# Optimization experiments

Measured on AMD Instinct MI355X. Metric: run time of the kernel, lower is better.

The kernel has to match this reference:

```python
import jax, jax.numpy as jnp
import numpy as np

B_TREES, NARY, HS, NHEAD, NLVL = 16, 3, 512, 2, 6
EDIM = 352
LN_EPS = 1e-5

def _build_structure():
    # forest of B_TREES perfect ternary trees, depth NLVL; nodes numbered leaves-first, level-major
    off, o = {}, 0
    for l in range(NLVL - 1, -1, -1):
        off[l] = o
        o += B_TREES * 3 ** l
    node_ids = [off[l] + np.arange(B_TREES * 3 ** l) for l in range(NLVL)]
    child_idx = {}
    for l in range(NLVL - 1):
        m = 3 ** l
        t = np.repeat(np.arange(B_TREES), m)
        p = np.tile(np.arange(m), B_TREES)
        base = off[l + 1] + t * (3 ** (l + 1)) + 3 * p
        child_idx[l] = base[:, None] + np.arange(NARY)[None, :]
    return o, node_ids, child_idx

N_NODES, NODE_IDS, CHILD_IDX = _build_structure()

def _ln(x, w, b):
    mu = x.mean(-1, keepdims=True)
    var = x.var(-1, keepdims=True)
    return (x - mu) / jnp.sqrt(var + LN_EPS) * w + b

def _mha(x, wqkv, bqkv, wo, bo):
    # x: [S, B, H]; torch MHA with batch_first=False (seq dim 0, as in reduce_func)
    S, B, H = x.shape
    hd = H // NHEAD
    q, k, v = jnp.split(x @ wqkv.T + bqkv, 3, axis=-1)
    q = q.reshape(S, B, NHEAD, hd)
    k = k.reshape(S, B, NHEAD, hd)
    v = v.reshape(S, B, NHEAD, hd)
    scores = jnp.einsum('sbnd,tbnd->bnst', q, k) / jnp.sqrt(jnp.asarray(hd, x.dtype))
    attn = jax.nn.softmax(scores, axis=-1)
    o = jnp.einsum('bnst,tbnd->sbnd', attn, v).reshape(S, B, H)
    return o @ wo.T + bo

def _transformer(x, qkv_w, qkv_b, out_w, out_b, ln1_w, ln1_b, ff1_w, ff1_b, ff2_w, ff2_b, ln2_w, ln2_b):
    # 2 post-norm TransformerEncoderLayers, relu FF, dropout off (eval)
    for i in range(2):
        x = _ln(x + _mha(x, qkv_w[i], qkv_b[i], out_w[i], out_b[i]), ln1_w[i], ln1_b[i])
        ff = jax.nn.relu(x @ ff1_w[i].T + ff1_b[i]) @ ff2_w[i].T + ff2_b[i]
        x = _ln(x + ff, ln2_w[i], ln2_b[i])
    return x

def _forward(floats, ints):
    (user_emb, poi_emb, cat_emb, coo_emb, time_pos, W_iou, U_iou, b_iou,
     W_f, U_f, b_f, qkv_w, qkv_b, out_w, out_b, ln1_w, ln1_b, ff1_w, ff1_b,
     ff2_w, ff2_b, ln2_w, ln2_b, dec_poi_w, dec_poi_b, dec_cat_w, dec_cat_b,
     dec_coo_w, dec_coo_b) = floats
    user_ids, poi_ids, cat_ids, coo_ids, time_ids, mask = ints
    mi = mask.astype(jnp.int32)
    x = jnp.concatenate([user_emb[user_ids * mi], poi_emb[poi_ids * mi],
                         cat_emb[cat_ids * mi], coo_emb[coo_ids * mi]], axis=1)
    x = x + 0.5 * time_pos[time_ids * mi]
    x = x * mask.astype(x.dtype)[:, None]  # embed_dropout is identity in eval; per-node mask
    h = jnp.zeros((N_NODES, HS), x.dtype)
    c = jnp.zeros((N_NODES, HS), x.dtype)
    # leaves: reduce never fires -> iou stays at W_iou(x) (no b_iou), c = 0
    leaf = NODE_IDS[NLVL - 1]
    i0, o0, u0 = jnp.split(x[leaf] @ W_iou.T, 3, axis=1)
    c_leaf = jax.nn.sigmoid(i0) * jnp.tanh(u0)
    h = h.at[leaf].set(jax.nn.sigmoid(o0) * jnp.tanh(c_leaf))
    c = c.at[leaf].set(c_leaf)
    # topological propagation, bottom-up level frontiers
    for l in range(NLVL - 2, -1, -1):
        idx = NODE_IDS[l]
        ci = CHILD_IDX[l]
        m = idx.shape[0]
        h_ch = h[ci]  # mailbox gather [m, nary, HS]
        c_ch = c[ci]
        xl = x[idx]
        Wx = jnp.tile(xl @ W_f.T, (1, NARY))
        f = jax.nn.sigmoid(Wx + h_ch.reshape(m, NARY * HS) @ U_f.T + jnp.tile(b_f, (1, NARY)))
        h_att = _transformer(h_ch, qkv_w, qkv_b, out_w, out_b, ln1_w, ln1_b,
                             ff1_w, ff1_b, ff2_w, ff2_b, ln2_w, ln2_b)
        iou = xl @ W_iou.T + h_att.reshape(m, NARY * HS) @ U_iou.T + b_iou
        c_red = jnp.sum(f.reshape(m, NARY, HS) * c_ch, axis=1)
        i1, o1, u1 = jnp.split(iou, 3, axis=1)
        c_new = jax.nn.sigmoid(i1) * jnp.tanh(u1) + c_red
        h_new = jax.nn.sigmoid(o1) * jnp.tanh(c_new)
        h = h.at[idx].set(h_new)
        c = c.at[idx].set(c_new)
    # model_dropout identity in eval
    y_poi = h @ dec_poi_w.T + dec_poi_b
    y_cat = h @ dec_cat_w.T + dec_cat_b
    y_coo = h @ dec_coo_w.T + dec_coo_b
    return y_poi, y_cat, y_coo

def setup_inputs():
    key = jax.random.key(0)
    ks = iter(jax.random.split(key, 64))
    def rn(shape, s=0.05):
        return jax.random.normal(next(ks), shape, dtype=jnp.float32) * s
    def ri(shape, hi):
        return jax.random.randint(next(ks), shape, 0, hi, dtype=jnp.int32)
    N = N_NODES
    return dict(
        user_ids=ri([N], 3000), poi_ids=ri([N], 5000), cat_ids=ri([N], 300),
        coo_ids=ri([N], 1024), time_ids=ri([N], 96), mask=ri([N], 2),
        user_emb=rn([3000, 128], 0.02), poi_emb=rn([5000, 128], 0.02),
        cat_emb=rn([300, 32], 0.02), coo_emb=rn([1024, 64], 0.02),
        time_pos=rn([96, EDIM], 0.02),
        W_iou=rn([3 * HS, EDIM]), U_iou=rn([3 * HS, NARY * HS]), b_iou=jnp.zeros((1, 3 * HS)),
        W_f=rn([HS, EDIM]), U_f=rn([NARY * HS, NARY * HS]), b_f=jnp.zeros((1, HS)),
        qkv_w=rn([2, 3 * HS, HS]), qkv_b=jnp.zeros((2, 3 * HS)),
        out_w=rn([2, HS, HS]), out_b=jnp.zeros((2, HS)),
        ln1_w=jnp.ones((2, HS)), ln1_b=jnp.zeros((2, HS)),
        ff1_w=rn([2, HS, HS]), ff1_b=jnp.zeros((2, HS)),
        ff2_w=rn([2, HS, HS]), ff2_b=jnp.zeros((2, HS)),
        ln2_w=jnp.ones((2, HS)), ln2_b=jnp.zeros((2, HS)),
        dec_poi_w=rn([5000, HS]), dec_poi_b=jnp.zeros((5000,)),
        dec_cat_w=rn([300, HS]), dec_cat_b=jnp.zeros((300,)),
        dec_coo_w=rn([1024, HS]), dec_coo_b=jnp.zeros((1024,)),
    )

def reference(user_ids, poi_ids, cat_ids, coo_ids, time_ids, mask,
              user_emb, poi_emb, cat_emb, coo_emb, time_pos,
              W_iou, U_iou, b_iou, W_f, U_f, b_f,
              qkv_w, qkv_b, out_w, out_b, ln1_w, ln1_b, ff1_w, ff1_b,
              ff2_w, ff2_b, ln2_w, ln2_b,
              dec_poi_w, dec_poi_b, dec_cat_w, dec_cat_b, dec_coo_w, dec_coo_b):
    floats = (user_emb, poi_emb, cat_emb, coo_emb, time_pos, W_iou, U_iou, b_iou,
              W_f, U_f, b_f, qkv_w, qkv_b, out_w, out_b, ln1_w, ln1_b, ff1_w, ff1_b,
              ff2_w, ff2_b, ln2_w, ln2_b, dec_poi_w, dec_poi_b, dec_cat_w, dec_cat_b,
              dec_coo_w, dec_coo_b)
    ints = (user_ids, poi_ids, cat_ids, coo_ids, time_ids, mask)
    return _forward(floats, ints)
```

## Files before the change

### kernel.cpp

```cpp
#include <hip/hip_runtime.h>
#include <hip/hip_bf16.h>


namespace {

constexpr int NN = 5824;
constexpr int ED = 352;

typedef __bf16 bf16;
typedef short s16x8 __attribute__((ext_vector_type(8)));
typedef float f32x4 __attribute__((ext_vector_type(4)));

__device__ __forceinline__ float sigmoidf_(float x) { return 1.f / (1.f + expf(-x)); }

__device__ __forceinline__ void gload_lds16(const void* g, void* s) {
  __builtin_amdgcn_global_load_lds(
      (const __attribute__((address_space(1))) unsigned int*)g,
      (__attribute__((address_space(3))) unsigned int*)s, 16, 0, 0);
}

template <int MODE>
__global__ __launch_bounds__(256) void bgemm_k(
    const bf16* __restrict__ A, const bf16* __restrict__ Alo, const bf16* __restrict__ B,
    void* __restrict__ Cp, bf16* __restrict__ Clo, const float* __restrict__ Cacc,
    const float* __restrict__ bias, int M, int N, int K, int lda, int ldb, int ldc,
    float alpha, long long sA1, long long sA2, long long sB1, long long sB2,
    long long sC1, long long sC2, int nh) {
  constexpr bool DUAL = (MODE == 1 || MODE == 2 || MODE == 4 || MODE == 5 || MODE == 6);
  const int bz = blockIdx.z;
  const int b1 = bz / nh, b2 = bz - b1 * nh;
  A += (long long)b1 * sA1 + (long long)b2 * sA2;
  if (DUAL) Alo += (long long)b1 * sA1 + (long long)b2 * sA2;
  B += (long long)b1 * sB1 + (long long)b2 * sB2;
  const long long coff = (long long)b1 * sC1 + (long long)b2 * sC2;
  const int bm = blockIdx.y * 128, bn = blockIdx.x * 128;
  __shared__ bf16 As[128 * 32];
  __shared__ bf16 Ls[DUAL ? 128 * 32 : 8];
  __shared__ bf16 Bs[128 * 32];
  const int tid = threadIdx.x;
  const int l = tid & 63;
  const int wr = ((tid >> 7) & 1) * 64;
  const int wc = ((tid >> 6) & 1) * 64;
  f32x4 acc[4][4];
#pragma unroll
  for (int i = 0; i < 4; ++i)
#pragma unroll
    for (int j = 0; j < 4; ++j) acc[i][j] = (f32x4){0.f, 0.f, 0.f, 0.f};

  for (int k0 = 0; k0 < K; k0 += 32) {
#pragma unroll
    for (int r = 0; r < 2; ++r) {
      int idx = r * 256 + tid;
      int row = idx >> 2, cs = idx & 3;
      int cg = cs ^ (row & 3);
      int ra = bm + row; if (ra > M - 1) ra = M - 1;
      int rb = bn + row; if (rb > N - 1) rb = N - 1;
      gload_lds16(A + (long long)ra * lda + k0 + cg * 8, As + idx * 8);
      if (DUAL) gload_lds16(Alo + (long long)ra * lda + k0 + cg * 8, Ls + idx * 8);
      gload_lds16(B + (long long)rb * ldb + k0 + cg * 8, Bs + idx * 8);
    }
    __syncthreads();
    s16x8 af[4], al[4], bfr[4];
#pragma unroll
    for (int mi = 0; mi < 4; ++mi) {
      int row = wr + mi * 16 + (l & 15);
      int ch = ((l >> 4) ^ row) & 3;
      af[mi] = *reinterpret_cast<const s16x8*>(As + row * 32 + ch * 8);
      if (DUAL) al[mi] = *reinterpret_cast<const s16x8*>(Ls + row * 32 + ch * 8);
    }
#pragma unroll
    for (int ni = 0; ni < 4; ++ni) {
      int row = wc + ni * 16 + (l & 15);
      int ch = ((l >> 4) ^ row) & 3;
      bfr[ni] = *reinterpret_cast<const s16x8*>(Bs + row * 32 + ch * 8);
    }
#pragma unroll
    for (int mi = 0; mi < 4; ++mi)
#pragma unroll
      for (int ni = 0; ni < 4; ++ni) {
        acc[mi][ni] =
            __builtin_amdgcn_mfma_f32_16x16x32_bf16(af[mi], bfr[ni], acc[mi][ni], 0, 0, 0);
        if (DUAL)
          acc[mi][ni] =
              __builtin_amdgcn_mfma_f32_16x16x32_bf16(al[mi], bfr[ni], acc[mi][ni], 0, 0, 0);
      }
    __syncthreads();
  }

  const int lc = l & 15, lr4 = (l >> 4) * 4;
#pragma unroll
  for (int mi = 0; mi < 4; ++mi) {
#pragma unroll
    for (int j = 0; j < 4; ++j) {
      int r = bm + wr + mi * 16 + lr4 + j;
      if (r >= M) continue;
#pragma unroll
      for (int ni = 0; ni < 4; ++ni) {
        int c = bn + wc + ni * 16 + lc;
        if (c >= N) continue;
        float v = alpha * acc[mi][ni][j];
        if (bias) v += bias[c];
        long long idx = coff + (long long)r * ldc + c;
        if (MODE == 5) v += Cacc[idx];
        if (MODE == 0 || MODE == 1 || MODE == 5) {
          ((float*)Cp)[idx] = v;
        } else if (MODE == 2 || MODE == 3) {
          ((bf16*)Cp)[idx] = (bf16)v;
        } else if (MODE == 4) {
          v = fmaxf(v, 0.f);
          bf16 hv = (bf16)v;
          ((bf16*)Cp)[idx] = hv;
          Clo[idx] = (bf16)(v - (float)hv);
        } else {
          float* o0 = (float*)Cp;
          if (c < 5000)      o0[(long long)r * 5000 + c] = v;
          else if (c < 5300) o0[29120000LL + (long long)r * 300 + (c - 5000)] = v;
          else               o0[30867200LL + (long long)r * 1024 + (c - 5300)] = v;
        }
      }
    }
  }
}

static void bgemm(hipStream_t st, int mode, const bf16* A, const bf16* Alo, const bf16* B,
                  void* Cp, bf16* Clo, const float* Cacc, const float* bias,
                  int M, int N, int K, int lda, int ldb, int ldc, float alpha,
                  int batches = 1, long long sA1 = 0, long long sA2 = 0, long long sB1 = 0,
                  long long sB2 = 0, long long sC1 = 0, long long sC2 = 0, int nh = 1) {
  dim3 g((N + 127) / 128, (M + 127) / 128, batches), b(256);
#define BGL(MD_)                                                                          \
  bgemm_k<MD_><<<g, b, 0, st>>>(A, Alo, B, Cp, Clo, Cacc, bias, M, N, K, lda, ldb, ldc,   \
                                alpha, sA1, sA2, sB1, sB2, sC1, sC2, nh)
  switch (mode) {
    case 0: BGL(0); break;
    case 1: BGL(1); break;
    case 2: BGL(2); break;
    case 3: BGL(3); break;
    case 4: BGL(4); break;
    case 5: BGL(5); break;
    default: BGL(6); break;
  }
#undef BGL
}

__global__ __launch_bounds__(256) void cvt8_k(const float* __restrict__ s,
                                              bf16* __restrict__ d, int n8) {
  int i = blockIdx.x * 256 + threadIdx.x;
  if (i >= n8) return;
  const float4* p = reinterpret_cast<const float4*>(s + (long long)i * 8);
  float4 a = p[0], b = p[1];
  bf16 o[8] = {(bf16)a.x, (bf16)a.y, (bf16)a.z, (bf16)a.w,
               (bf16)b.x, (bf16)b.y, (bf16)b.z, (bf16)b.w};
  *reinterpret_cast<s16x8*>(d + (long long)i * 8) = *reinterpret_cast<s16x8*>(o);
}

__global__ __launch_bounds__(256) void biascat_k(const float* __restrict__ p,
                                                 const float* __restrict__ c,
                                                 const float* __restrict__ g,
                                                 float* __restrict__ o) {
  int i = blockIdx.x * 256 + threadIdx.x;
  if (i >= 6324) return;
  o[i] = (i < 5000) ? p[i] : (i < 5300) ? c[i - 5000] : g[i - 5300];
}

__global__ __launch_bounds__(256) void embed_k(
    const int* __restrict__ uid, const int* __restrict__ pid, const int* __restrict__ cid,
    const int* __restrict__ gid, const int* __restrict__ tmid, const int* __restrict__ mask,
    const float* __restrict__ ue, const float* __restrict__ pe, const float* __restrict__ ce,
    const float* __restrict__ ge, const float* __restrict__ tp, bf16* __restrict__ xb) {
  int e = blockIdx.x * 256 + threadIdx.x;
  if (e >= NN * ED) return;
  int n = e / ED, j = e - n * ED;
  int mi = mask[n];
  float fm = (float)mi;
  float v;
  if (j < 128)      v = ue[(long long)(uid[n] * mi) * 128 + j];
  else if (j < 256) v = pe[(long long)(pid[n] * mi) * 128 + (j - 128)];
  else if (j < 288) v = ce[(long long)(cid[n] * mi) * 32 + (j - 256)];
  else              v = ge[(long long)(gid[n] * mi) * 64 + (j - 288)];
  v += 0.5f * tp[(long long)(tmid[n] * mi) * ED + j];
  xb[e] = (bf16)(v * fm);
}

__global__ __launch_bounds__(256) void gather_k(
    const bf16* __restrict__ hhi, const bf16* __restrict__ hlo, const float* __restrict__ c,
    bf16* __restrict__ ghi, bf16* __restrict__ glo, float* __restrict__ cch,
    int m, int cbase, int tl) {
  int e = blockIdx.x * 256 + threadIdx.x;
  if (e >= m * 1536) return;
  int r = e / 1536, rem = e - r * 1536;
  int k = rem >> 9, d = rem & 511;
  int t = r / tl, p = r - t * tl;
  long long src = (long long)(cbase + t * 3 * tl + 3 * p + k) * 512 + d;
  ghi[e] = hhi[src];
  glo[e] = hlo[src];
  cch[e] = c[src];
}

__global__ __launch_bounds__(256) void fcred_k(
    const float* __restrict__ wx, const float* __restrict__ ufh, const float* __restrict__ bf_,
    const float* __restrict__ cch, float* __restrict__ cred, int m) {
  int e = blockIdx.x * 256 + threadIdx.x;
  if (e >= m * 512) return;
  int r = e >> 9, d = e & 511;
  float w = wx[e] + bf_[d];
  long long base = (long long)r * 1536;
  float acc = 0.f;
#pragma unroll
  for (int k = 0; k < 3; ++k) {
    float f = sigmoidf_(w + ufh[base + k * 512 + d]);
    acc += f * cch[base + k * 512 + d];
  }
  cred[e] = acc;
}

__global__ __launch_bounds__(256) void combine_k(
    const float* __restrict__ iou, const float* __restrict__ cred, float* __restrict__ c,
    bf16* __restrict__ hhi, bf16* __restrict__ hlo, int off, int m) {
  int e = blockIdx.x * 256 + threadIdx.x;
  if (e >= m * 512) return;
  int r = e >> 9, d = e & 511;
  long long b = (long long)r * 1536;
  float iv = iou[b + d], ov = iou[b + 512 + d], uv = iou[b + 1024 + d];
  float cr = cred ? cred[e] : 0.f;
  float cn = sigmoidf_(iv) * tanhf(uv) + cr;
  float hn = sigmoidf_(ov) * tanhf(cn);
  long long o = (long long)(off + r) * 512 + d;
  c[o] = cn;
  bf16 hv = (bf16)hn;
  hhi[o] = hv;
  hlo[o] = (bf16)(hn - (float)hv);
}

__global__ __launch_bounds__(256) void ln_k(
    const bf16* __restrict__ ahi, const bf16* __restrict__ alo, const float* __restrict__ b,
    const float* __restrict__ w, const float* __restrict__ bias,
    bf16* __restrict__ ohi, bf16* __restrict__ olo) {
  int r = blockIdx.x, t = threadIdx.x;
  long long base = (long long)r * 512;
  float v0 = (float)ahi[base + t] + (float)alo[base + t] + b[base + t];
  float v1 = (float)ahi[base + 256 + t] + (float)alo[base + 256 + t] + b[base + 256 + t];
  __shared__ float s1[256], s2[256];
  s1[t] = v0 + v1;
  s2[t] = v0 * v0 + v1 * v1;
  __syncthreads();
  for (int s = 128; s > 0; s >>= 1) {
    if (t < s) { s1[t] += s1[t + s]; s2[t] += s2[t + s]; }
    __syncthreads();
  }
  float mu = s1[0] * (1.f / 512.f);
  float var = s2[0] * (1.f / 512.f) - mu * mu;
  float rs = rsqrtf(var + 1e-5f);
  float o0 = (v0 - mu) * rs * w[t] + bias[t];
  float o1 = (v1 - mu) * rs * w[256 + t] + bias[256 + t];
  bf16 h0 = (bf16)o0, h1 = (bf16)o1;
  ohi[base + t] = h0;       olo[base + t] = (bf16)(o0 - (float)h0);
  ohi[base + 256 + t] = h1; olo[base + 256 + t] = (bf16)(o1 - (float)h1);
}

__global__ __launch_bounds__(256) void softmax_pb_k(
    const float* __restrict__ sc, bf16* __restrict__ pb, int m, int mpad) {
  long long r = blockIdx.x;
  const float* row = sc + r * m;
  bf16* prow = pb + r * mpad;
  int t = threadIdx.x;
  __shared__ float sh[256];
  float mx = -3.4e38f;
  for (int j = t; j < m; j += 256) mx = fmaxf(mx, row[j]);
  sh[t] = mx;
  __syncthreads();
  for (int s = 128; s > 0; s >>= 1) {
    if (t < s) sh[t] = fmaxf(sh[t], sh[t + s]);
    __syncthreads();
  }
  mx = sh[0];
  __syncthreads();
  float sum = 0.f;
  for (int j = t; j < m; j += 256) sum += expf(row[j] - mx);
  sh[t] = sum;
  __syncthreads();
  for (int s = 128; s > 0; s >>= 1) {
    if (t < s) sh[t] += sh[t + s];
    __syncthreads();
  }
  float inv = 1.f / sh[0];
  for (int j = t; j < mpad; j += 256)
    prow[j] = (j < m) ? (bf16)(expf(row[j] - mx) * inv) : (bf16)0.f;
}

__global__ __launch_bounds__(256) void vt_k(const bf16* __restrict__ qkvb,
                                            bf16* __restrict__ vt, int m, int mpad) {
  int total = 6 * 256 * mpad;
  for (int e = blockIdx.x * 256 + threadIdx.x; e < total; e += gridDim.x * 256) {
    int z = e / (256 * mpad);
    int rem = e - z * 256 * mpad;
    int n = rem / mpad, k = rem - n * mpad;
    int b = z >> 1, h = z & 1;
    bf16 v = (bf16)0.f;
    if (k < m) v = qkvb[(long long)(k * 3 + b) * 1536 + 1024 + h * 256 + n];
    vt[e] = v;
  }
}

}

extern "C" void kernel_launch(void* const* d_in, const int* in_sizes, int n_in,
                              void* d_out, int out_size, void* d_ws, size_t ws_size,
                              hipStream_t stream) {
  const int* uid  = (const int*)d_in[0];
  const int* pid  = (const int*)d_in[1];
  const int* cid  = (const int*)d_in[2];
  const int* gid  = (const int*)d_in[3];
  const int* tmid = (const int*)d_in[4];
  const int* mask = (const int*)d_in[5];
  const float* ue = (const float*)d_in[6];
  const float* pe = (const float*)d_in[7];
  const float* ce = (const float*)d_in[8];
  const float* ge = (const float*)d_in[9];
  const float* tp = (const float*)d_in[10];
  const float* W_iou = (const float*)d_in[11];
  const float* U_iou = (const float*)d_in[12];
  const float* b_iou = (const float*)d_in[13];
  const float* W_f = (const float*)d_in[14];
  const float* U_f = (const float*)d_in[15];
  const float* b_f = (const float*)d_in[16];
  const float* qkv_w = (const float*)d_in[17];
  const float* qkv_b = (const float*)d_in[18];
  const float* out_w = (const float*)d_in[19];
  const float* out_b = (const float*)d_in[20];
  const float* ln1_w = (const float*)d_in[21];
  const float* ln1_b = (const float*)d_in[22];
  const float* ff1_w = (const float*)d_in[23];
  const float* ff1_b = (const float*)d_in[24];
  const float* ff2_w = (const float*)d_in[25];
  const float* ff2_b = (const float*)d_in[26];
  const float* ln2_w = (const float*)d_in[27];
  const float* ln2_b = (const float*)d_in[28];
  const float* dpw = (const float*)d_in[29];
  const float* dpb = (const float*)d_in[30];
  const float* dcw = (const float*)d_in[31];
  const float* dcb = (const float*)d_in[32];
  const float* dgw = (const float*)d_in[33];
  const float* dgb = (const float*)d_in[34];

  float* ws = (float*)d_ws;
  bf16* Hhi = (bf16*)ws;
  bf16* Hlo = Hhi + 2981888LL;
  bf16* dwcat = (bf16*)(ws + 2981888LL);
  float* bcat = ws + 4600832LL;

  float* ob = (float*)d_out;
  float* R1   = ob;
  float* PQ   = ob + 10077696LL;
  bf16* VT    = (bf16*)(ob + 15178752LL);
  bf16* ATTOb = (bf16*)(ob + 16186368LL);
  float* SCR  = ob + 17181696LL;
  bf16* XChi  = (bf16*)(ob + 19172352LL);
  bf16* XClo  = XChi + 1990656LL;
  bf16* RAhi  = (bf16*)(ob + 21163008LL);
  bf16* RAlo  = RAhi + 1990656LL;
  bf16* RBhi  = (bf16*)(ob + 23153664LL);
  bf16* RBlo  = RBhi + 1990656LL;
  float* WX   = ob + 25144320LL;
  float* CRED = ob + 25807872LL;
  float* Cc   = ob + 26471424LL;
  bf16* Xb    = (bf16*)(ob + 29453312LL);
  bf16* Wb    = (bf16*)(ob + 30478336LL);

  float* SC   = R1;
  float* IOU  = R1;
  bf16* QKVb  = (bf16*)PQ;
  float* UFH  = PQ;
  bf16* Pb    = (bf16*)PQ;
  float* CCH  = SCR;
  float* XB   = SCR;

  bf16* W_ioub = Wb;
  bf16* U_ioub = Wb + 540672LL;
  bf16* W_fb   = Wb + 2899968LL;
  bf16* U_fb   = Wb + 3080192LL;
  bf16* qkvb   = Wb + 5439488LL;
  bf16* outb   = Wb + 7012352LL;
  bf16* ff1b   = Wb + 7536640LL;
  bf16* ff2b   = Wb + 8060928LL;

#define CVT(src, dst, n) cvt8_k<<<((n) / 8 + 255) / 256, 256, 0, stream>>>(src, dst, (n) / 8)
  CVT(W_iou, W_ioub, 540672);
  CVT(U_iou, U_ioub, 2359296);
  CVT(W_f, W_fb, 180224);
  CVT(U_f, U_fb, 2359296);
  CVT(qkv_w, qkvb, 1572864);
  CVT(out_w, outb, 524288);
  CVT(ff1_w, ff1b, 524288);
  CVT(ff2_w, ff2b, 524288);
  CVT(dpw, dwcat, 2560000);
  CVT(dcw, dwcat + 2560000LL, 153600);
  CVT(dgw, dwcat + 2713600LL, 524288);
#undef CVT
  biascat_k<<<25, 256, 0, stream>>>(dpb, dcb, dgb, bcat);

  embed_k<<<(NN * ED + 255) / 256, 256, 0, stream>>>(uid, pid, cid, gid, tmid, mask,
                                                     ue, pe, ce, ge, tp, Xb);

  bgemm(stream, 0, Xb, nullptr, W_ioub, R1, nullptr, nullptr, nullptr,
        3888, 1536, 352, 352, 352, 1536, 1.f);
  combine_k<<<(3888 * 512 + 255) / 256, 256, 0, stream>>>(R1, nullptr, Cc, Hhi, Hlo, 0, 3888);

  static const int OFFL[6] = {5808, 5760, 5616, 5184, 3888, 0};
  int tl = 81;
  for (int l = 4; l >= 0; --l, tl /= 3) {
    int m = 16 * tl;
    int off = OFFL[l];
    int cbase = OFFL[l + 1];
    int T = 3 * m;
    int mpad = (m + 31) & ~31;
    const bf16* xlb = Xb + (long long)off * ED;

    gather_k<<<(m * 1536 + 255) / 256, 256, 0, stream>>>(Hhi, Hlo, Cc, RAhi, RAlo, CCH,
                                                         m, cbase, tl);
    bgemm(stream, 0, xlb, nullptr, W_fb, WX, nullptr, nullptr, nullptr,
          m, 512, 352, 352, 352, 512, 1.f);
    bgemm(stream, 1, RAhi, RAlo, U_fb, UFH, nullptr, nullptr, nullptr,
          m, 1536, 1536, 1536, 1536, 1536, 1.f);
    fcred_k<<<(m * 512 + 255) / 256, 256, 0, stream>>>(WX, UFH, b_f, CCH, CRED, m);

    bf16 *curhi = RAhi, *curlo = RAlo, *nxthi = RBhi, *nxtlo = RBlo;
    for (int i = 0; i < 2; ++i) {
      bgemm(stream, 2, curhi, curlo, qkvb + (long long)i * 786432, QKVb, nullptr, nullptr,
            qkv_b + i * 1536, T, 1536, 512, 512, 512, 1536, 1.f);
      {
        int total = 6 * 256 * mpad;
        int blocks = (total + 255) / 256; if (blocks > 2048) blocks = 2048;
        vt_k<<<blocks, 256, 0, stream>>>(QKVb, VT, m, mpad);
      }
      bgemm(stream, 0, QKVb, nullptr, QKVb + 512, SC, nullptr, nullptr, nullptr,
            m, m, 256, 4608, 4608, m, 0.0625f,
            6, 1536, 256, 1536, 256, 2LL * m * m, (long long)m * m, 2);
      softmax_pb_k<<<6 * m, 256, 0, stream>>>(SC, Pb, m, mpad);
      bgemm(stream, 3, Pb, nullptr, VT, ATTOb, nullptr, nullptr, nullptr,
            m, 256, mpad, mpad, mpad, 1536, 1.f,
            6, 2LL * m * mpad, (long long)m * mpad, 2LL * 256 * mpad, 256LL * mpad,
            512, 256, 2);
      bgemm(stream, 0, ATTOb, nullptr, outb + (long long)i * 262144, XB, nullptr, nullptr,
            out_b + i * 512, T, 512, 512, 512, 512, 512, 1.f);
      ln_k<<<T, 256, 0, stream>>>(curhi, curlo, XB, ln1_w + i * 512, ln1_b + i * 512,
                                  nxthi, nxtlo);
      bgemm(stream, 4, nxthi, nxtlo, ff1b + (long long)i * 262144, XChi, XClo, nullptr,
            ff1_b + i * 512, T, 512, 512, 512, 512, 512, 1.f);
      bgemm(stream, 1, XChi, XClo, ff2b + (long long)i * 262144, XB, nullptr, nullptr,
            ff2_b + i * 512, T, 512, 512, 512, 512, 512, 1.f);
      ln_k<<<T, 256, 0, stream>>>(nxthi, nxtlo, XB, ln2_w + i * 512, ln2_b + i * 512,
                                  curhi, curlo);
    }

    bgemm(stream, 0, xlb, nullptr, W_ioub, IOU, nullptr, nullptr, b_iou,
          m, 1536, 352, 352, 352, 1536, 1.f);
    bgemm(stream, 5, curhi, curlo, U_ioub, IOU, nullptr, IOU, nullptr,
          m, 1536, 1536, 1536, 1536, 1536, 1.f);
    combine_k<<<(m * 512 + 255) / 256, 256, 0, stream>>>(IOU, CRED, Cc, Hhi, Hlo, off, m);
  }

  bgemm(stream, 6, Hhi, Hlo, dwcat, ob, nullptr, nullptr, bcat,
        NN, 6324, 512, 512, 512, 0, 1.f);
}
```

Before: 2.417 ms.

## Convert fp32 weights inside GEMM tiles and fuse gather, V-transpose and batched projections

Drops the upfront weight conversion kernels. The GEMM now loads fp32 weights directly and splits them into hi/lo bf16 pairs, adding an extra MFMA per step for weight precision. The V transpose moves into the QKV GEMM epilogue, child gathering moves into combine_k and fcred_k, and the W_iou/W_f input projections run once for all nodes instead of per level. The decoder reads its three weight and bias tables directly, removing concatenation. This cuts launches and intermediate traffic, but the extra MFMAs and in-loop fp32 conversion add compute on every GEMM, including the large decoder GEMM.

```diff
diff --git a/kernel.cpp b/kernel.cpp
--- a/kernel.cpp
+++ b/kernel.cpp
@@ -19,24 +19,31 @@
       (__attribute__((address_space(3))) unsigned int*)s, 16, 0, 0);
 }
 
-template <int MODE>
+template <int MODE, int BSRC>
 __global__ __launch_bounds__(256) void bgemm_k(
-    const bf16* __restrict__ A, const bf16* __restrict__ Alo, const bf16* __restrict__ B,
+    const bf16* __restrict__ A, const bf16* __restrict__ Alo,
+    const bf16* __restrict__ Bb, const float* __restrict__ Bf,
+    const float* __restrict__ Bf0, const float* __restrict__ Bf1,
+    const float* __restrict__ Bf2,
     void* __restrict__ Cp, bf16* __restrict__ Clo, const float* __restrict__ Cacc,
-    const float* __restrict__ bias, int M, int N, int K, int lda, int ldb, int ldc,
-    float alpha, long long sA1, long long sA2, long long sB1, long long sB2,
+    const float* __restrict__ bias, const float* __restrict__ bias1,
+    const float* __restrict__ bias2, bf16* __restrict__ VTout, int mpad,
+    int M, int N, int K, int lda, int ldb, int ldc, float alpha,
+    long long sA1, long long sA2, long long sB1, long long sB2,
     long long sC1, long long sC2, int nh) {
-  constexpr bool DUAL = (MODE == 1 || MODE == 2 || MODE == 4 || MODE == 5 || MODE == 6);
+  constexpr bool DUAL = (MODE == 1 || MODE == 4 || MODE == 5 || MODE == 6 || MODE == 7);
+  constexpr bool WF = (BSRC >= 1);
   const int bz = blockIdx.z;
   const int b1 = bz / nh, b2 = bz - b1 * nh;
   A += (long long)b1 * sA1 + (long long)b2 * sA2;
   if (DUAL) Alo += (long long)b1 * sA1 + (long long)b2 * sA2;
-  B += (long long)b1 * sB1 + (long long)b2 * sB2;
+  if (BSRC == 0) Bb += (long long)b1 * sB1 + (long long)b2 * sB2;
   const long long coff = (long long)b1 * sC1 + (long long)b2 * sC2;
   const int bm = blockIdx.y * 128, bn = blockIdx.x * 128;
   __shared__ bf16 As[128 * 32];
   __shared__ bf16 Ls[DUAL ? 128 * 32 : 8];
-  __shared__ bf16 Bs[128 * 32];
+  __shared__ bf16 Bh[128 * 32];
+  __shared__ bf16 Bl[WF ? 128 * 32 : 8];
   const int tid = threadIdx.x;
   const int l = tid & 63;
   const int wr = ((tid >> 7) & 1) * 64;
@@ -57,10 +64,33 @@
       int rb = bn + row; if (rb > N - 1) rb = N - 1;
       gload_lds16(A + (long long)ra * lda + k0 + cg * 8, As + idx * 8);
       if (DUAL) gload_lds16(Alo + (long long)ra * lda + k0 + cg * 8, Ls + idx * 8);
-      gload_lds16(B + (long long)rb * ldb + k0 + cg * 8, Bs + idx * 8);
+      if (BSRC == 0) {
+        gload_lds16(Bb + (long long)rb * ldb + k0 + cg * 8, Bh + idx * 8);
+      } else {
+        const float* src;
+        if (BSRC == 2) {
+          if (rb < 5000)      src = Bf0 + (long long)rb * ldb + k0 + cg * 8;
+          else if (rb < 5300) src = Bf1 + (long long)(rb - 5000) * ldb + k0 + cg * 8;
+          else                src = Bf2 + (long long)(rb - 5300) * ldb + k0 + cg * 8;
+        } else {
+          src = Bf + (long long)rb * ldb + k0 + cg * 8;
+        }
+        float4 x = *reinterpret_cast<const float4*>(src);
+        float4 y = *reinterpret_cast<const float4*>(src + 4);
+        float w[8] = {x.x, x.y, x.z, x.w, y.x, y.y, y.z, y.w};
+        bf16 hb_[8], lb_[8];
+#pragma unroll
+        for (int q = 0; q < 8; ++q) {
+          bf16 hq = (bf16)w[q];
+          hb_[q] = hq;
+          lb_[q] = (bf16)(w[q] - (float)hq);
+        }
+        *reinterpret_cast<s16x8*>(Bh + idx * 8) = *reinterpret_cast<s16x8*>(hb_);
+        *reinterpret_cast<s16x8*>(Bl + idx * 8) = *reinterpret_cast<s16x8*>(lb_);
+      }
     }
     __syncthreads();
-    s16x8 af[4], al[4], bfr[4];
+    s16x8 af[4], al[4], bh[4], bl2[4];
 #pragma unroll
     for (int mi = 0; mi < 4; ++mi) {
       int row = wr + mi * 16 + (l & 15);
@@ -72,17 +102,21 @@
     for (int ni = 0; ni < 4; ++ni) {
       int row = wc + ni * 16 + (l & 15);
       int ch = ((l >> 4) ^ row) & 3;
-      bfr[ni] = *reinterpret_cast<const s16x8*>(Bs + row * 32 + ch * 8);
+      bh[ni] = *reinterpret_cast<const s16x8*>(Bh + row * 32 + ch * 8);
+      if (WF) bl2[ni] = *reinterpret_cast<const s16x8*>(Bl + row * 32 + ch * 8);
     }
 #pragma unroll
     for (int mi = 0; mi < 4; ++mi)
 #pragma unroll
       for (int ni = 0; ni < 4; ++ni) {
         acc[mi][ni] =
-            __builtin_amdgcn_mfma_f32_16x16x32_bf16(af[mi], bfr[ni], acc[mi][ni], 0, 0, 0);
+            __builtin_amdgcn_mfma_f32_16x16x32_bf16(af[mi], bh[ni], acc[mi][ni], 0, 0, 0);
+        if (WF)
+          acc[mi][ni] =
+              __builtin_amdgcn_mfma_f32_16x16x32_bf16(af[mi], bl2[ni], acc[mi][ni], 0, 0, 0);
         if (DUAL)
           acc[mi][ni] =
-              __builtin_amdgcn_mfma_f32_16x16x32_bf16(al[mi], bfr[ni], acc[mi][ni], 0, 0, 0);
+              __builtin_amdgcn_mfma_f32_16x16x32_bf16(al[mi], bh[ni], acc[mi][ni], 0, 0, 0);
       }
     __syncthreads();
   }
@@ -93,18 +127,31 @@
 #pragma unroll
     for (int j = 0; j < 4; ++j) {
       int r = bm + wr + mi * 16 + lr4 + j;
-      if (r >= M) continue;
+      if (MODE != 7 && r >= M) continue;
 #pragma unroll
       for (int ni = 0; ni < 4; ++ni) {
         int c = bn + wc + ni * 16 + lc;
         if (c >= N) continue;
         float v = alpha * acc[mi][ni][j];
-        if (bias) v += bias[c];
+        if (MODE == 6) {
+          v += (c < 5000) ? bias[c] : (c < 5300) ? bias1[c - 5000] : bias2[c - 5300];
+        } else if (bias) {
+          v += bias[c];
+        }
         long long idx = coff + (long long)r * ldc + c;
-        if (MODE == 5) v += Cacc[idx];
-        if (MODE == 0 || MODE == 1 || MODE == 5) {
+        if (MODE == 7) {
+          if (c >= 1024 && r < 3 * mpad) {
+            bf16 pv = (r < M) ? (bf16)v : (bf16)0.f;
+            int r3 = r % 3, s = r / 3;
+            int hh = (c - 1024) >> 8, n = (c - 1024) & 255;
+            VTout[(long long)((r3 * 2 + hh) * 256 + n) * mpad + s] = pv;
+          }
+          if (r < M) ((bf16*)Cp)[idx] = (bf16)v;
+        } else if (MODE == 5) {
+          ((float*)Cp)[idx] = v + Cacc[idx];
+        } else if (MODE == 0 || MODE == 1) {
           ((float*)Cp)[idx] = v;
-        } else if (MODE == 2 || MODE == 3) {
+        } else if (MODE == 3) {
           ((bf16*)Cp)[idx] = (bf16)v;
         } else if (MODE == 4) {
           v = fmaxf(v, 0.f);
@@ -122,45 +169,37 @@
   }
 }
 
-static void bgemm(hipStream_t st, int mode, const bf16* A, const bf16* Alo, const bf16* B,
-                  void* Cp, bf16* Clo, const float* Cacc, const float* bias,
+static void bgemm(hipStream_t st, int mode, int bsrc,
+                  const bf16* A, const bf16* Alo,
+                  const bf16* Bb, const float* Bf,
+                  const float* Bf0, const float* Bf1, const float* Bf2,
+                  void* Cp, bf16* Clo, const float* Cacc,
+                  const float* bias, const float* bias1, const float* bias2,
+                  bf16* VTout, int mpad,
                   int M, int N, int K, int lda, int ldb, int ldc, float alpha,
-                  int batches = 1, long long sA1 = 0, long long sA2 = 0, long long sB1 = 0,
-                  long long sB2 = 0, long long sC1 = 0, long long sC2 = 0, int nh = 1) {
+                  int batches = 1, long long sA1 = 0, long long sA2 = 0,
+                  long long sB1 = 0, long long sB2 = 0, long long sC1 = 0,
+                  long long sC2 = 0, int nh = 1) {
   dim3 g((N + 127) / 128, (M + 127) / 128, batches), b(256);
-#define BGL(MD_)                                                                          \
-  bgemm_k<MD_><<<g, b, 0, st>>>(A, Alo, B, Cp, Clo, Cacc, bias, M, N, K, lda, ldb, ldc,   \
-                                alpha, sA1, sA2, sB1, sB2, sC1, sC2, nh)
-  switch (mode) {
-    case 0: BGL(0); break;
-    case 1: BGL(1); break;
-    case 2: BGL(2); break;
-    case 3: BGL(3); break;
-    case 4: BGL(4); break;
-    case 5: BGL(5); break;
-    default: BGL(6); break;
+#define BGL(MD_, BS_)                                                                \
+  bgemm_k<MD_, BS_><<<g, b, 0, st>>>(A, Alo, Bb, Bf, Bf0, Bf1, Bf2, Cp, Clo, Cacc,   \
+                                     bias, bias1, bias2, VTout, mpad, M, N, K, lda,  \
+                                     ldb, ldc, alpha, sA1, sA2, sB1, sB2, sC1, sC2, nh)
+  if (bsrc == 0) {
+    if (mode == 0) BGL(0, 0);
+    else           BGL(3, 0);
+  } else if (bsrc == 2) {
+    BGL(6, 2);
+  } else {
+    switch (mode) {
+      case 0: BGL(0, 1); break;
+      case 1: BGL(1, 1); break;
+      case 4: BGL(4, 1); break;
+      case 5: BGL(5, 1); break;
+      default: BGL(7, 1); break;
+    }
   }
 #undef BGL
-}
-
-__global__ __launch_bounds__(256) void cvt8_k(const float* __restrict__ s,
-                                              bf16* __restrict__ d, int n8) {
-  int i = blockIdx.x * 256 + threadIdx.x;
-  if (i >= n8) return;
-  const float4* p = reinterpret_cast<const float4*>(s + (long long)i * 8);
-  float4 a = p[0], b = p[1];
-  bf16 o[8] = {(bf16)a.x, (bf16)a.y, (bf16)a.z, (bf16)a.w,
-               (bf16)b.x, (bf16)b.y, (bf16)b.z, (bf16)b.w};
-  *reinterpret_cast<s16x8*>(d + (long long)i * 8) = *reinterpret_cast<s16x8*>(o);
-}
-
-__global__ __launch_bounds__(256) void biascat_k(const float* __restrict__ p,
-                                                 const float* __restrict__ c,
-                                                 const float* __restrict__ g,
-                                                 float* __restrict__ o) {
-  int i = blockIdx.x * 256 + threadIdx.x;
-  if (i >= 6324) return;
-  o[i] = (i < 5000) ? p[i] : (i < 5300) ? c[i - 5000] : g[i - 5300];
 }
 
 __global__ __launch_bounds__(256) void embed_k(
@@ -182,41 +221,30 @@
   xb[e] = (bf16)(v * fm);
 }
 
-__global__ __launch_bounds__(256) void gather_k(
-    const bf16* __restrict__ hhi, const bf16* __restrict__ hlo, const float* __restrict__ c,
-    bf16* __restrict__ ghi, bf16* __restrict__ glo, float* __restrict__ cch,
-    int m, int cbase, int tl) {
-  int e = blockIdx.x * 256 + threadIdx.x;
-  if (e >= m * 1536) return;
-  int r = e / 1536, rem = e - r * 1536;
-  int k = rem >> 9, d = rem & 511;
-  int t = r / tl, p = r - t * tl;
-  long long src = (long long)(cbase + t * 3 * tl + 3 * p + k) * 512 + d;
-  ghi[e] = hhi[src];
-  glo[e] = hlo[src];
-  cch[e] = c[src];
-}
-
 __global__ __launch_bounds__(256) void fcred_k(
-    const float* __restrict__ wx, const float* __restrict__ ufh, const float* __restrict__ bf_,
-    const float* __restrict__ cch, float* __restrict__ cred, int m) {
+    const float* __restrict__ wxa, const float* __restrict__ ufh,
+    const float* __restrict__ bf_, const float* __restrict__ c, float* __restrict__ cred,
+    int m, int cbase, int tl, int woff) {
   int e = blockIdx.x * 256 + threadIdx.x;
   if (e >= m * 512) return;
   int r = e >> 9, d = e & 511;
-  float w = wx[e] + bf_[d];
-  long long base = (long long)r * 1536;
+  float w = wxa[(long long)(woff + r) * 512 + d] + bf_[d];
+  int t = r / tl, p = r - t * tl;
+  long long cb = (long long)(cbase + t * 3 * tl + 3 * p) * 512 + d;
+  long long ub = (long long)r * 1536;
   float acc = 0.f;
 #pragma unroll
   for (int k = 0; k < 3; ++k) {
-    float f = sigmoidf_(w + ufh[base + k * 512 + d]);
-    acc += f * cch[base + k * 512 + d];
+    float f = sigmoidf_(w + ufh[ub + k * 512 + d]);
+    acc += f * c[cb + (long long)k * 512];
   }
   cred[e] = acc;
 }
 
 __global__ __launch_bounds__(256) void combine_k(
     const float* __restrict__ iou, const float* __restrict__ cred, float* __restrict__ c,
-    bf16* __restrict__ hhi, bf16* __restrict__ hlo, int off, int m) {
+    bf16* __restrict__ hhi, bf16* __restrict__ hlo, int off, int m, int tl3, int tlp,
+    bf16* __restrict__ nxthi, bf16* __restrict__ nxtlo) {
   int e = blockIdx.x * 256 + threadIdx.x;
   if (e >= m * 512) return;
   int r = e >> 9, d = e & 511;
@@ -228,8 +256,16 @@
   long long o = (long long)(off + r) * 512 + d;
   c[o] = cn;
   bf16 hv = (bf16)hn;
+  bf16 lo = (bf16)(hn - (float)hv);
   hhi[o] = hv;
-  hlo[o] = (bf16)(hn - (float)hv);
+  hlo[o] = lo;
+  if (nxthi) {
+    int t = r / tl3, q = r - t * tl3;
+    int qp = q / 3, slot = q - 3 * qp;
+    long long dst = (long long)(t * tlp + qp) * 1536 + slot * 512 + d;
+    nxthi[dst] = hv;
+    nxtlo[dst] = lo;
+  }
 }
 
 __global__ __launch_bounds__(256) void ln_k(
@@ -286,20 +322,6 @@
   float inv = 1.f / sh[0];
   for (int j = t; j < mpad; j += 256)
     prow[j] = (j < m) ? (bf16)(expf(row[j] - mx) * inv) : (bf16)0.f;
-}
-
-__global__ __launch_bounds__(256) void vt_k(const bf16* __restrict__ qkvb,
-                                            bf16* __restrict__ vt, int m, int mpad) {
-  int total = 6 * 256 * mpad;
-  for (int e = blockIdx.x * 256 + threadIdx.x; e < total; e += gridDim.x * 256) {
-    int z = e / (256 * mpad);
-    int rem = e - z * 256 * mpad;
-    int n = rem / mpad, k = rem - n * mpad;
-    int b = z >> 1, h = z & 1;
-    bf16 v = (bf16)0.f;
-    if (k < m) v = qkvb[(long long)(k * 3 + b) * 1536 + 1024 + h * 256 + n];
-    vt[e] = v;
-  }
 }
 
 }
@@ -346,65 +368,42 @@
   float* ws = (float*)d_ws;
   bf16* Hhi = (bf16*)ws;
   bf16* Hlo = Hhi + 2981888LL;
-  bf16* dwcat = (bf16*)(ws + 2981888LL);
-  float* bcat = ws + 4600832LL;
+  float* Cc = ws + 2981888LL;
 
   float* ob = (float*)d_out;
-  float* R1   = ob;
-  float* PQ   = ob + 10077696LL;
-  bf16* VT    = (bf16*)(ob + 15178752LL);
-  bf16* ATTOb = (bf16*)(ob + 16186368LL);
-  float* SCR  = ob + 17181696LL;
-  bf16* XChi  = (bf16*)(ob + 19172352LL);
-  bf16* XClo  = XChi + 1990656LL;
-  bf16* RAhi  = (bf16*)(ob + 21163008LL);
+  float* IOUa = ob;
+  float* WXa  = ob + 8945664LL;
+  float* CRED = ob + 9936896LL;
+  bf16* RAhi  = (bf16*)(ob + 10600448LL);
   bf16* RAlo  = RAhi + 1990656LL;
-  bf16* RBhi  = (bf16*)(ob + 23153664LL);
+  bf16* RBhi  = (bf16*)(ob + 12591104LL);
   bf16* RBlo  = RBhi + 1990656LL;
-  float* WX   = ob + 25144320LL;
-  float* CRED = ob + 25807872LL;
-  float* Cc   = ob + 26471424LL;
-  bf16* Xb    = (bf16*)(ob + 29453312LL);
-  bf16* Wb    = (bf16*)(ob + 30478336LL);
-
-  float* SC   = R1;
-  float* IOU  = R1;
-  bf16* QKVb  = (bf16*)PQ;
-  float* UFH  = PQ;
-  bf16* Pb    = (bf16*)PQ;
-  float* CCH  = SCR;
-  float* XB   = SCR;
-
-  bf16* W_ioub = Wb;
-  bf16* U_ioub = Wb + 540672LL;
-  bf16* W_fb   = Wb + 2899968LL;
-  bf16* U_fb   = Wb + 3080192LL;
-  bf16* qkvb   = Wb + 5439488LL;
-  bf16* outb   = Wb + 7012352LL;
-  bf16* ff1b   = Wb + 7536640LL;
-  bf16* ff2b   = Wb + 8060928LL;
-
-#define CVT(src, dst, n) cvt8_k<<<((n) / 8 + 255) / 256, 256, 0, stream>>>(src, dst, (n) / 8)
-  CVT(W_iou, W_ioub, 540672);
-  CVT(U_iou, U_ioub, 2359296);
-  CVT(W_f, W_fb, 180224);
-  CVT(U_f, U_fb, 2359296);
-  CVT(qkv_w, qkvb, 1572864);
-  CVT(out_w, outb, 524288);
-  CVT(ff1_w, ff1b, 524288);
-  CVT(ff2_w, ff2b, 524288);
-  CVT(dpw, dwcat, 2560000);
-  CVT(dcw, dwcat + 2560000LL, 153600);
-  CVT(dgw, dwcat + 2713600LL, 524288);
-#undef CVT
-  biascat_k<<<25, 256, 0, stream>>>(dpb, dcb, dgb, bcat);
+  bf16* Xb    = (bf16*)(ob + 14581760LL);
+  float* TB   = ob + 15606784LL;
+  float* SC   = TB;
+  bf16* ATTOb = (bf16*)TB;
+  float* XB   = TB + 995328LL;
+  bf16* XChi  = (bf16*)(TB + 2985984LL);
+  bf16* XClo  = (bf16*)(TB + 3981312LL);
+  float* PQ   = TB + 10077696LL;
+  bf16* VT    = (bf16*)(TB + 15178752LL);
+
+  float* UFH = PQ;
+  bf16* QKVb = (bf16*)PQ;
+  bf16* Pb   = (bf16*)PQ;
 
   embed_k<<<(NN * ED + 255) / 256, 256, 0, stream>>>(uid, pid, cid, gid, tmid, mask,
                                                      ue, pe, ce, ge, tp, Xb);
 
-  bgemm(stream, 0, Xb, nullptr, W_ioub, R1, nullptr, nullptr, nullptr,
-        3888, 1536, 352, 352, 352, 1536, 1.f);
-  combine_k<<<(3888 * 512 + 255) / 256, 256, 0, stream>>>(R1, nullptr, Cc, Hhi, Hlo, 0, 3888);
+  bgemm(stream, 0, 1, Xb, nullptr, nullptr, W_iou, nullptr, nullptr, nullptr,
+        IOUa, nullptr, nullptr, nullptr, nullptr, nullptr, nullptr, 0,
+        NN, 1536, 352, 352, 352, 1536, 1.f);
+  bgemm(stream, 0, 1, Xb + 3888LL * ED, nullptr, nullptr, W_f, nullptr, nullptr, nullptr,
+        WXa, nullptr, nullptr, nullptr, nullptr, nullptr, nullptr, 0,
+        1936, 512, 352, 352, 352, 512, 1.f);
+
+  combine_k<<<(3888 * 512 + 255) / 256, 256, 0, stream>>>(
+      IOUa, nullptr, Cc, Hhi, Hlo, 0, 3888, 243, 81, RAhi, RAlo);
 
   static const int OFFL[6] = {5808, 5760, 5616, 5184, 3888, 0};
   int tl = 81;
@@ -414,52 +413,57 @@
     int cbase = OFFL[l + 1];
     int T = 3 * m;
     int mpad = (m + 31) & ~31;
-    const bf16* xlb = Xb + (long long)off * ED;
-
-    gather_k<<<(m * 1536 + 255) / 256, 256, 0, stream>>>(Hhi, Hlo, Cc, RAhi, RAlo, CCH,
-                                                         m, cbase, tl);
-    bgemm(stream, 0, xlb, nullptr, W_fb, WX, nullptr, nullptr, nullptr,
-          m, 512, 352, 352, 352, 512, 1.f);
-    bgemm(stream, 1, RAhi, RAlo, U_fb, UFH, nullptr, nullptr, nullptr,
+
+    bgemm(stream, 1, 1, RAhi, RAlo, nullptr, U_f, nullptr, nullptr, nullptr,
+          UFH, nullptr, nullptr, nullptr, nullptr, nullptr, nullptr, 0,
           m, 1536, 1536, 1536, 1536, 1536, 1.f);
-    fcred_k<<<(m * 512 + 255) / 256, 256, 0, stream>>>(WX, UFH, b_f, CCH, CRED, m);
+    fcred_k<<<(m * 512 + 255) / 256, 256, 0, stream>>>(WXa, UFH, b_f, Cc, CRED,
+                                                       m, cbase, tl, off - 3888);
 
     bf16 *curhi = RAhi, *curlo = RAlo, *nxthi = RBhi, *nxtlo = RBlo;
     for (int i = 0; i < 2; ++i) {
-      bgemm(stream, 2, curhi, curlo, qkvb + (long long)i * 786432, QKVb, nullptr, nullptr,
-            qkv_b + i * 1536, T, 1536, 512, 512, 512, 1536, 1.f);
-      {
-        int total = 6 * 256 * mpad;
-        int blocks = (total + 255) / 256; if (blocks > 2048) blocks = 2048;
-        vt_k<<<blocks, 256, 0, stream>>>(QKVb, VT, m, mpad);
-      }
-      bgemm(stream, 0, QKVb, nullptr, QKVb + 512, SC, nullptr, nullptr, nullptr,
+      bgemm(stream, 7, 1, curhi, curlo, nullptr, qkv_w + (long long)i * 786432,
+            nullptr, nullptr, nullptr, QKVb, nullptr, nullptr,
+            qkv_b + i * 1536, nullptr, nullptr, VT, mpad,
+            T, 1536, 512, 512, 512, 1536, 1.f);
+      bgemm(stream, 0, 0, QKVb, nullptr, QKVb + 512, nullptr, nullptr, nullptr, nullptr,
+            SC, nullptr, nullptr, nullptr, nullptr, nullptr, nullptr, 0,
             m, m, 256, 4608, 4608, m, 0.0625f,
             6, 1536, 256, 1536, 256, 2LL * m * m, (long long)m * m, 2);
       softmax_pb_k<<<6 * m, 256, 0, stream>>>(SC, Pb, m, mpad);
-      bgemm(stream, 3, Pb, nullptr, VT, ATTOb, nullptr, nullptr, nullptr,
+      bgemm(stream, 3, 0, Pb, nullptr, VT, nullptr, nullptr, nullptr, nullptr,
+            ATTOb, nullptr, nullptr, nullptr, nullptr, nullptr, nullptr, 0,
             m, 256, mpad, mpad, mpad, 1536, 1.f,
             6, 2LL * m * mpad, (long long)m * mpad, 2LL * 256 * mpad, 256LL * mpad,
             512, 256, 2);
-      bgemm(stream, 0, ATTOb, nullptr, outb + (long long)i * 262144, XB, nullptr, nullptr,
-            out_b + i * 512, T, 512, 512, 512, 512, 512, 1.f);
+      bgemm(stream, 0, 1, ATTOb, nullptr, nullptr, out_w + (long long)i * 262144,
+            nullptr, nullptr, nullptr, XB, nullptr, nullptr,
+            out_b + i * 512, nullptr, nullptr, nullptr, 0,
+            T, 512, 512, 512, 512, 512, 1.f);
       ln_k<<<T, 256, 0, stream>>>(curhi, curlo, XB, ln1_w + i * 512, ln1_b + i * 512,
                                   nxthi, nxtlo);
-      bgemm(stream, 4, nxthi, nxtlo, ff1b + (long long)i * 262144, XChi, XClo, nullptr,
-            ff1_b + i * 512, T, 512, 512, 512, 512, 512, 1.f);
-      bgemm(stream, 1, XChi, XClo, ff2b + (long long)i * 262144, XB, nullptr, nullptr,
-            ff2_b + i * 512, T, 512, 512, 512, 512, 512, 1.f);
+      bgemm(stream, 4, 1, nxthi, nxtlo, nullptr, ff1_w + (long long)i * 262144,
+            nullptr, nullptr, nullptr, XChi, XClo, nullptr,
+            ff1_b + i * 512, nullptr, nullptr, nullptr, 0,
+            T, 512, 512, 512, 512, 512, 1.f);
+      bgemm(stream, 1, 1, XChi, XClo, nullptr, ff2_w + (long long)i * 262144,
+            nullptr, nullptr, nullptr, XB, nullptr, nullptr,
+            ff2_b + i * 512, nullptr, nullptr, nullptr, 0,
+            T, 512, 512, 512, 512, 512, 1.f);
       ln_k<<<T, 256, 0, stream>>>(nxthi, nxtlo, XB, ln2_w + i * 512, ln2_b + i * 512,
                                   curhi, curlo);
     }
 
-    bgemm(stream, 0, xlb, nullptr, W_ioub, IOU, nullptr, nullptr, b_iou,
-          m, 1536, 352, 352, 352, 1536, 1.f);
-    bgemm(stream, 5, curhi, curlo, U_ioub, IOU, nullptr, IOU, nullptr,
+    bgemm(stream, 5, 1, curhi, curlo, nullptr, U_iou, nullptr, nullptr, nullptr,
+          IOUa + (long long)off * 1536, nullptr, IOUa + (long long)off * 1536,
+          b_iou, nullptr, nullptr, nullptr, 0,
           m, 1536, 1536, 1536, 1536, 1536, 1.f);
-    combine_k<<<(m * 512 + 255) / 256, 256, 0, stream>>>(IOU, CRED, Cc, Hhi, Hlo, off, m);
-  }
-
-  bgemm(stream, 6, Hhi, Hlo, dwcat, ob, nullptr, nullptr, bcat,
+    combine_k<<<(m * 512 + 255) / 256, 256, 0, stream>>>(
+        IOUa + (long long)off * 1536, CRED, Cc, Hhi, Hlo, off, m, tl, tl / 3,
+        l > 0 ? RAhi : nullptr, l > 0 ? RAlo : nullptr);
+  }
+
+  bgemm(stream, 6, 2, Hhi, Hlo, nullptr, nullptr, dpw, dcw, dgw,
+        ob, nullptr, nullptr, dpb, dcb, dgb, nullptr, 0,
         NN, 6324, 512, 512, 512, 0, 1.f);
 }
```

Result: slower. 2.818 ms (+16.6%).
